# Performance work log

Hardware: AMD Instinct MI355X
Metric: run time of the kernel (lower is better)

## Reference

```python
import jax, jax.numpy as jnp
import numpy as np

NUM_HEADS = 8
HIDDEN_DIM = 64
N_REAL = 30000
N_VIRT = 2000
N_NODES = N_REAL + N_VIRT
N_EDGES = 512000
VOCAB = 100000


def setup_inputs() -> dict:
    key = jax.random.key(0)
    k1, k2, k3, k4, k5 = jax.random.split(key, 5)
    features = jax.random.normal(k1, (VOCAB, HIDDEN_DIM), dtype=jnp.float32)
    virtue_emb = jax.random.normal(k2, (N_VIRT, HIDDEN_DIM), dtype=jnp.float32)  # nn.Embedding weight ~ N(0,1)
    cnodes = jax.random.randint(k3, (N_REAL,), 0, VOCAB, dtype=jnp.int64)
    src = jax.random.randint(k4, (N_EDGES,), 0, N_NODES, dtype=jnp.int64)
    dst = jax.random.randint(k5, (N_EDGES,), 0, N_NODES, dtype=jnp.int64)
    vm_idx = jnp.arange(N_VIRT, dtype=jnp.int64) + N_REAL  # virtual nodes are appended after real nodes
    return {"features": features, "virtue_emb": virtue_emb, "cnodes": cnodes,
            "src": src, "dst": dst, "vm_idx": vm_idx}


def _edge_softmax(e, dst, n_nodes):
    # DGL edge_softmax: softmax over incoming edges of each destination node.
    m = jax.ops.segment_max(e, dst, num_segments=n_nodes)          # [N,H,1]
    ex = jnp.exp(e - m[dst])                                       # [E,H,1]
    s = jax.ops.segment_sum(ex, dst, num_segments=n_nodes)        # [N,H,1]
    return ex / s[dst]


def reference(features, virtue_emb, cnodes, src, dst, vm_idx):
    real_ndata = features[cnodes]                                  # [R,D] F.embedding
    ndata = jnp.concatenate([real_ndata, virtue_emb], axis=0)      # [N,D]
    n = ndata.shape[0]
    # agg_type='neighbor': cat([h]*H, dim=1).view(-1,H,D) == broadcast along head dim
    nft = jnp.broadcast_to(ndata[:, None, :], (n, NUM_HEADS, HIDDEN_DIM))
    e = jnp.ones((src.shape[0], NUM_HEADS, 1), dtype=ndata.dtype)
    eft = _edge_softmax(e, dst, n)                                 # [E,H,1]
    new_nft = jax.ops.segment_sum(nft[src] * eft, dst, num_segments=n)      # round 1: u_mul_e / sum
    final_nft = jax.ops.segment_sum(new_nft[src] * eft, dst, num_segments=n)  # round 2
    return final_nft[vm_idx]                                       # [V,H,D]
```

## Files before the change

### kernel.cpp

```cpp
#include <hip/hip_runtime.h>

constexpr int HEADS  = 8;
constexpr int DIM    = 64;
constexpr int NREAL  = 30000;
constexpr int NVIRT  = 2000;
constexpr int NNODES = NREAL + NVIRT;
constexpr int NEDGES = 512000;
constexpr int STRIDE = 64;

typedef _Float16 half4 __attribute__((ext_vector_type(4)));


__global__ __launch_bounds__(256) void k_prep(const float* __restrict__ features,
                                              const float* __restrict__ virtue,
                                              const int* __restrict__ cnodes,
                                              const int* __restrict__ src,
                                              const int* __restrict__ dst,
                                              _Float16* __restrict__ ndata,
                                              int* __restrict__ cnt,
                                              unsigned char* __restrict__ mark,
                                              unsigned short* __restrict__ slots) {
  int i = blockIdx.x * blockDim.x + threadIdx.x;
  {
    int node = i >> 4;
    int q    = i & 15;
    const float4* srcp = (node < NREAL)
        ? (const float4*)(features + (long)cnodes[node] * DIM)
        : (const float4*)(virtue + (long)(node - NREAL) * DIM);
    float4 v = srcp[q];
    half4 h = { (_Float16)v.x, (_Float16)v.y, (_Float16)v.z, (_Float16)v.w };
    ((half4*)(ndata + (long)node * DIM))[q] = h;
  }
  {
    int d = dst[i];
    int s = src[i];
    int pos = atomicAdd(&cnt[d], 1);
    if (pos < STRIDE) slots[(long)d * STRIDE + pos] = (unsigned short)s;
    if (d >= NREAL) mark[s] = 1;
  }
}

__global__ __launch_bounds__(256) void k_agg1(const int* __restrict__ cnt,
                                              const unsigned char* __restrict__ mark,
                                              const unsigned short* __restrict__ slots,
                                              const _Float16* __restrict__ ndata,
                                              float* __restrict__ new_nft) {
  int node = blockIdx.x * 4 + (threadIdx.x >> 6);
  if (node >= NNODES) return;
  if (!mark[node]) return;
  int lane = threadIdx.x & 63;
  int q = lane >> 4;
  int l = lane & 15;
  int deg = cnt[node];
  if (deg > STRIDE) deg = STRIDE;
  int myidx = 0;
  if (lane < deg) myidx = (int)slots[(long)node * STRIDE + lane];
  float4 acc  = make_float4(0.f, 0.f, 0.f, 0.f);
  float4 acc2 = make_float4(0.f, 0.f, 0.f, 0.f);
  const half4* nd = (const half4*)ndata;
  for (int k0 = 0; k0 < deg; k0 += 8) {
    int ka = k0 + q;
    int kb = k0 + q + 4;
    int sa = __shfl(myidx, ka);
    int sb = __shfl(myidx, kb);
    if (ka < deg) {
      half4 v = nd[(long)sa * 16 + l];
      acc.x += (float)v.x; acc.y += (float)v.y; acc.z += (float)v.z; acc.w += (float)v.w;
    }
    if (kb < deg) {
      half4 v = nd[(long)sb * 16 + l];
      acc2.x += (float)v.x; acc2.y += (float)v.y; acc2.z += (float)v.z; acc2.w += (float)v.w;
    }
  }
  acc.x += acc2.x; acc.y += acc2.y; acc.z += acc2.z; acc.w += acc2.w;
  acc.x += __shfl_xor(acc.x, 16); acc.y += __shfl_xor(acc.y, 16);
  acc.z += __shfl_xor(acc.z, 16); acc.w += __shfl_xor(acc.w, 16);
  acc.x += __shfl_xor(acc.x, 32); acc.y += __shfl_xor(acc.y, 32);
  acc.z += __shfl_xor(acc.z, 32); acc.w += __shfl_xor(acc.w, 32);
  if (q == 0) {
    float inv = (deg > 0) ? 1.0f / (float)deg : 0.0f;
    acc.x *= inv; acc.y *= inv; acc.z *= inv; acc.w *= inv;
    ((float4*)new_nft)[(long)node * 16 + l] = acc;
  }
}

__global__ __launch_bounds__(256) void k_agg2(const int* __restrict__ cnt,
                                              const unsigned short* __restrict__ slots,
                                              const float* __restrict__ new_nft,
                                              float* __restrict__ out) {
  int v = blockIdx.x * 4 + (threadIdx.x >> 6);
  if (v >= NVIRT) return;
  int node = NREAL + v;
  int lane = threadIdx.x & 63;
  int q = lane >> 4;
  int l = lane & 15;
  int deg = cnt[node];
  if (deg > STRIDE) deg = STRIDE;
  int myidx = 0;
  if (lane < deg) myidx = (int)slots[(long)node * STRIDE + lane];
  float4 acc  = make_float4(0.f, 0.f, 0.f, 0.f);
  float4 acc2 = make_float4(0.f, 0.f, 0.f, 0.f);
  const float4* nf4 = (const float4*)new_nft;
  for (int k0 = 0; k0 < deg; k0 += 8) {
    int ka = k0 + q;
    int kb = k0 + q + 4;
    int sa = __shfl(myidx, ka);
    int sb = __shfl(myidx, kb);
    if (ka < deg) {
      float4 x = nf4[(long)sa * 16 + l];
      acc.x += x.x; acc.y += x.y; acc.z += x.z; acc.w += x.w;
    }
    if (kb < deg) {
      float4 x = nf4[(long)sb * 16 + l];
      acc2.x += x.x; acc2.y += x.y; acc2.z += x.z; acc2.w += x.w;
    }
  }
  acc.x += acc2.x; acc.y += acc2.y; acc.z += acc2.z; acc.w += acc2.w;
  acc.x += __shfl_xor(acc.x, 16); acc.y += __shfl_xor(acc.y, 16);
  acc.z += __shfl_xor(acc.z, 16); acc.w += __shfl_xor(acc.w, 16);
  acc.x += __shfl_xor(acc.x, 32); acc.y += __shfl_xor(acc.y, 32);
  acc.z += __shfl_xor(acc.z, 32); acc.w += __shfl_xor(acc.w, 32);
  if (q == 0) {
    float inv = (deg > 0) ? 1.0f / (float)deg : 0.0f;
    acc.x *= inv; acc.y *= inv; acc.z *= inv; acc.w *= inv;
    float4* o4 = (float4*)out;
#pragma unroll
    for (int h = 0; h < HEADS; ++h)
      o4[((long)v * HEADS + h) * 16 + l] = acc;
  }
}


extern "C" void kernel_launch(void* const* d_in, const int* in_sizes, int n_in,
                              void* d_out, int out_size, void* d_ws, size_t ws_size,
                              hipStream_t stream) {
  const float* features = (const float*)d_in[0];
  const float* virtue   = (const float*)d_in[1];
  const int*   cnodes   = (const int*)d_in[2];
  const int*   src      = (const int*)d_in[3];
  const int*   dst      = (const int*)d_in[4];
  float* out = (float*)d_out;

  float*          new_nft = (float*)d_ws;
  _Float16*       ndata   = (_Float16*)(new_nft + (long)NNODES * DIM);
  int*            cnt     = (int*)(ndata + (long)NNODES * DIM);
  unsigned char*  mark    = (unsigned char*)(cnt + NNODES);
  unsigned short* slots   = (unsigned short*)(mark + NNODES);

  const int B = 256;

  hipMemsetAsync(cnt, 0, NNODES * sizeof(int) + NNODES, stream);
  k_prep<<<NEDGES / B, B, 0, stream>>>(features, virtue, cnodes, src, dst,
                                       ndata, cnt, mark, slots);
  k_agg1<<<(NNODES + 3) / 4, B, 0, stream>>>(cnt, mark, slots, ndata, new_nft);
  k_agg2<<<(NVIRT + 3) / 4, B, 0, stream>>>(cnt, slots, new_nft, out);
}
```

Measured before the change: 128.8 us.

## Fuse memset and three kernels into one cooperative persistent kernel

Replaces the memset and three separate launches with a single cooperative kernel of 1024 blocks that uses grid-wide syncs between the zeroing, prep/bucketing, first-aggregation and second-aggregation phases, with grid-stride loops in each phase. This removes launch overhead and the gaps between kernels. In exchange it adds three grid barriers, limits parallelism to a fixed resident grid, and makes the cooperative launch depend on all blocks being co-resident.

```diff
diff --git a/kernel.cpp b/kernel.cpp
--- a/kernel.cpp
+++ b/kernel.cpp
@@ -1,4 +1,7 @@
 #include <hip/hip_runtime.h>
+#include <hip/hip_cooperative_groups.h>
+
+namespace cg = cooperative_groups;
 
 constexpr int HEADS  = 8;
 constexpr int DIM    = 64;
@@ -8,125 +11,130 @@
 constexpr int NEDGES = 512000;
 constexpr int STRIDE = 64;
 
+constexpr int GRID = 1024;
+
 typedef _Float16 half4 __attribute__((ext_vector_type(4)));
 
+__global__ __launch_bounds__(256, 4) void k_fused(const float* __restrict__ features,
+                                                  const float* __restrict__ virtue,
+                                                  const int* __restrict__ cnodes,
+                                                  const int* __restrict__ src,
+                                                  const int* __restrict__ dst,
+                                                  _Float16* __restrict__ ndata,
+                                                  int* __restrict__ cnt,
+                                                  unsigned char* __restrict__ mark,
+                                                  unsigned short* __restrict__ slots,
+                                                  float* __restrict__ new_nft,
+                                                  float* __restrict__ out) {
+  cg::grid_group grid = cg::this_grid();
+  const int tid = blockIdx.x * blockDim.x + threadIdx.x;
+  const int nthreads = GRID * 256;
 
-__global__ __launch_bounds__(256) void k_prep(const float* __restrict__ features,
-                                              const float* __restrict__ virtue,
-                                              const int* __restrict__ cnodes,
-                                              const int* __restrict__ src,
-                                              const int* __restrict__ dst,
-                                              _Float16* __restrict__ ndata,
-                                              int* __restrict__ cnt,
-                                              unsigned char* __restrict__ mark,
-                                              unsigned short* __restrict__ slots) {
-  int i = blockIdx.x * blockDim.x + threadIdx.x;
-  {
-    int node = i >> 4;
-    int q    = i & 15;
-    const float4* srcp = (node < NREAL)
-        ? (const float4*)(features + (long)cnodes[node] * DIM)
-        : (const float4*)(virtue + (long)(node - NREAL) * DIM);
-    float4 v = srcp[q];
-    half4 h = { (_Float16)v.x, (_Float16)v.y, (_Float16)v.z, (_Float16)v.w };
-    ((half4*)(ndata + (long)node * DIM))[q] = h;
+  for (int i = tid; i < NNODES; i += nthreads) {
+    cnt[i] = 0;
+    mark[i] = 0;
   }
-  {
-    int d = dst[i];
-    int s = src[i];
-    int pos = atomicAdd(&cnt[d], 1);
-    if (pos < STRIDE) slots[(long)d * STRIDE + pos] = (unsigned short)s;
-    if (d >= NREAL) mark[s] = 1;
-  }
-}
+  grid.sync();
 
-__global__ __launch_bounds__(256) void k_agg1(const int* __restrict__ cnt,
-                                              const unsigned char* __restrict__ mark,
-                                              const unsigned short* __restrict__ slots,
-                                              const _Float16* __restrict__ ndata,
-                                              float* __restrict__ new_nft) {
-  int node = blockIdx.x * 4 + (threadIdx.x >> 6);
-  if (node >= NNODES) return;
-  if (!mark[node]) return;
-  int lane = threadIdx.x & 63;
-  int q = lane >> 4;
-  int l = lane & 15;
-  int deg = cnt[node];
-  if (deg > STRIDE) deg = STRIDE;
-  int myidx = 0;
-  if (lane < deg) myidx = (int)slots[(long)node * STRIDE + lane];
-  float4 acc  = make_float4(0.f, 0.f, 0.f, 0.f);
-  float4 acc2 = make_float4(0.f, 0.f, 0.f, 0.f);
-  const half4* nd = (const half4*)ndata;
-  for (int k0 = 0; k0 < deg; k0 += 8) {
-    int ka = k0 + q;
-    int kb = k0 + q + 4;
-    int sa = __shfl(myidx, ka);
-    int sb = __shfl(myidx, kb);
-    if (ka < deg) {
-      half4 v = nd[(long)sa * 16 + l];
-      acc.x += (float)v.x; acc.y += (float)v.y; acc.z += (float)v.z; acc.w += (float)v.w;
+  for (int i = tid; i < NEDGES; i += nthreads) {
+    {
+      int node = i >> 4;
+      int q    = i & 15;
+      const float4* srcp = (node < NREAL)
+          ? (const float4*)(features + (long)cnodes[node] * DIM)
+          : (const float4*)(virtue + (long)(node - NREAL) * DIM);
+      float4 v = srcp[q];
+      half4 h = { (_Float16)v.x, (_Float16)v.y, (_Float16)v.z, (_Float16)v.w };
+      ((half4*)(ndata + (long)node * DIM))[q] = h;
     }
-    if (kb < deg) {
-      half4 v = nd[(long)sb * 16 + l];
-      acc2.x += (float)v.x; acc2.y += (float)v.y; acc2.z += (float)v.z; acc2.w += (float)v.w;
+    {
+      int d = dst[i];
+      int s = src[i];
+      int pos = atomicAdd(&cnt[d], 1);
+      if (pos < STRIDE) slots[(long)d * STRIDE + pos] = (unsigned short)s;
+      if (d >= NREAL) mark[s] = 1;
     }
   }
-  acc.x += acc2.x; acc.y += acc2.y; acc.z += acc2.z; acc.w += acc2.w;
-  acc.x += __shfl_xor(acc.x, 16); acc.y += __shfl_xor(acc.y, 16);
-  acc.z += __shfl_xor(acc.z, 16); acc.w += __shfl_xor(acc.w, 16);
-  acc.x += __shfl_xor(acc.x, 32); acc.y += __shfl_xor(acc.y, 32);
-  acc.z += __shfl_xor(acc.z, 32); acc.w += __shfl_xor(acc.w, 32);
-  if (q == 0) {
-    float inv = (deg > 0) ? 1.0f / (float)deg : 0.0f;
-    acc.x *= inv; acc.y *= inv; acc.z *= inv; acc.w *= inv;
-    ((float4*)new_nft)[(long)node * 16 + l] = acc;
-  }
-}
+  grid.sync();
 
-__global__ __launch_bounds__(256) void k_agg2(const int* __restrict__ cnt,
-                                              const unsigned short* __restrict__ slots,
-                                              const float* __restrict__ new_nft,
-                                              float* __restrict__ out) {
-  int v = blockIdx.x * 4 + (threadIdx.x >> 6);
-  if (v >= NVIRT) return;
-  int node = NREAL + v;
-  int lane = threadIdx.x & 63;
-  int q = lane >> 4;
-  int l = lane & 15;
-  int deg = cnt[node];
-  if (deg > STRIDE) deg = STRIDE;
-  int myidx = 0;
-  if (lane < deg) myidx = (int)slots[(long)node * STRIDE + lane];
-  float4 acc  = make_float4(0.f, 0.f, 0.f, 0.f);
-  float4 acc2 = make_float4(0.f, 0.f, 0.f, 0.f);
-  const float4* nf4 = (const float4*)new_nft;
-  for (int k0 = 0; k0 < deg; k0 += 8) {
-    int ka = k0 + q;
-    int kb = k0 + q + 4;
-    int sa = __shfl(myidx, ka);
-    int sb = __shfl(myidx, kb);
-    if (ka < deg) {
-      float4 x = nf4[(long)sa * 16 + l];
-      acc.x += x.x; acc.y += x.y; acc.z += x.z; acc.w += x.w;
+  const int wave   = tid >> 6;
+  const int nwaves = nthreads >> 6;
+  const int lane   = threadIdx.x & 63;
+  const int q = lane >> 4;
+  const int l = lane & 15;
+
+  for (int node = wave; node < NNODES; node += nwaves) {
+    if (!mark[node]) continue;
+    int deg = cnt[node];
+    if (deg > STRIDE) deg = STRIDE;
+    int myidx = 0;
+    if (lane < deg) myidx = (int)slots[(long)node * STRIDE + lane];
+    float4 acc  = make_float4(0.f, 0.f, 0.f, 0.f);
+    float4 acc2 = make_float4(0.f, 0.f, 0.f, 0.f);
+    const half4* nd = (const half4*)ndata;
+    for (int k0 = 0; k0 < deg; k0 += 8) {
+      int ka = k0 + q;
+      int kb = k0 + q + 4;
+      int sa = __shfl(myidx, ka);
+      int sb = __shfl(myidx, kb);
+      if (ka < deg) {
+        half4 v = nd[(long)sa * 16 + l];
+        acc.x += (float)v.x; acc.y += (float)v.y; acc.z += (float)v.z; acc.w += (float)v.w;
+      }
+      if (kb < deg) {
+        half4 v = nd[(long)sb * 16 + l];
+        acc2.x += (float)v.x; acc2.y += (float)v.y; acc2.z += (float)v.z; acc2.w += (float)v.w;
+      }
     }
-    if (kb < deg) {
-      float4 x = nf4[(long)sb * 16 + l];
-      acc2.x += x.x; acc2.y += x.y; acc2.z += x.z; acc2.w += x.w;
+    acc.x += acc2.x; acc.y += acc2.y; acc.z += acc2.z; acc.w += acc2.w;
+    acc.x += __shfl_xor(acc.x, 16); acc.y += __shfl_xor(acc.y, 16);
+    acc.z += __shfl_xor(acc.z, 16); acc.w += __shfl_xor(acc.w, 16);
+    acc.x += __shfl_xor(acc.x, 32); acc.y += __shfl_xor(acc.y, 32);
+    acc.z += __shfl_xor(acc.z, 32); acc.w += __shfl_xor(acc.w, 32);
+    if (q == 0) {
+      float inv = (deg > 0) ? 1.0f / (float)deg : 0.0f;
+      acc.x *= inv; acc.y *= inv; acc.z *= inv; acc.w *= inv;
+      ((float4*)new_nft)[(long)node * 16 + l] = acc;
     }
   }
-  acc.x += acc2.x; acc.y += acc2.y; acc.z += acc2.z; acc.w += acc2.w;
-  acc.x += __shfl_xor(acc.x, 16); acc.y += __shfl_xor(acc.y, 16);
-  acc.z += __shfl_xor(acc.z, 16); acc.w += __shfl_xor(acc.w, 16);
-  acc.x += __shfl_xor(acc.x, 32); acc.y += __shfl_xor(acc.y, 32);
-  acc.z += __shfl_xor(acc.z, 32); acc.w += __shfl_xor(acc.w, 32);
-  if (q == 0) {
-    float inv = (deg > 0) ? 1.0f / (float)deg : 0.0f;
-    acc.x *= inv; acc.y *= inv; acc.z *= inv; acc.w *= inv;
-    float4* o4 = (float4*)out;
+  grid.sync();
+
+  for (int v = wave; v < NVIRT; v += nwaves) {
+    int node = NREAL + v;
+    int deg = cnt[node];
+    if (deg > STRIDE) deg = STRIDE;
+    int myidx = 0;
+    if (lane < deg) myidx = (int)slots[(long)node * STRIDE + lane];
+    float4 acc  = make_float4(0.f, 0.f, 0.f, 0.f);
+    float4 acc2 = make_float4(0.f, 0.f, 0.f, 0.f);
+    const float4* nf4 = (const float4*)new_nft;
+    for (int k0 = 0; k0 < deg; k0 += 8) {
+      int ka = k0 + q;
+      int kb = k0 + q + 4;
+      int sa = __shfl(myidx, ka);
+      int sb = __shfl(myidx, kb);
+      if (ka < deg) {
+        float4 x = nf4[(long)sa * 16 + l];
+        acc.x += x.x; acc.y += x.y; acc.z += x.z; acc.w += x.w;
+      }
+      if (kb < deg) {
+        float4 x = nf4[(long)sb * 16 + l];
+        acc2.x += x.x; acc2.y += x.y; acc2.z += x.z; acc2.w += x.w;
+      }
+    }
+    acc.x += acc2.x; acc.y += acc2.y; acc.z += acc2.z; acc.w += acc2.w;
+    acc.x += __shfl_xor(acc.x, 16); acc.y += __shfl_xor(acc.y, 16);
+    acc.z += __shfl_xor(acc.z, 16); acc.w += __shfl_xor(acc.w, 16);
+    acc.x += __shfl_xor(acc.x, 32); acc.y += __shfl_xor(acc.y, 32);
+    acc.z += __shfl_xor(acc.z, 32); acc.w += __shfl_xor(acc.w, 32);
+    if (q == 0) {
+      float inv = (deg > 0) ? 1.0f / (float)deg : 0.0f;
+      acc.x *= inv; acc.y *= inv; acc.z *= inv; acc.w *= inv;
+      float4* o4 = (float4*)out;
 #pragma unroll
-    for (int h = 0; h < HEADS; ++h)
-      o4[((long)v * HEADS + h) * 16 + l] = acc;
+      for (int h = 0; h < HEADS; ++h)
+        o4[((long)v * HEADS + h) * 16 + l] = acc;
+    }
   }
 }
 
@@ -147,11 +155,8 @@
   unsigned char*  mark    = (unsigned char*)(cnt + NNODES);
   unsigned short* slots   = (unsigned short*)(mark + NNODES);
 
-  const int B = 256;
-
-  hipMemsetAsync(cnt, 0, NNODES * sizeof(int) + NNODES, stream);
-  k_prep<<<NEDGES / B, B, 0, stream>>>(features, virtue, cnodes, src, dst,
-                                       ndata, cnt, mark, slots);
-  k_agg1<<<(NNODES + 3) / 4, B, 0, stream>>>(cnt, mark, slots, ndata, new_nft);
-  k_agg2<<<(NVIRT + 3) / 4, B, 0, stream>>>(cnt, slots, new_nft, out);
+  void* args[] = { (void*)&features, (void*)&virtue, (void*)&cnodes, (void*)&src,
+                   (void*)&dst, (void*)&ndata, (void*)&cnt, (void*)&mark,
+                   (void*)&slots, (void*)&new_nft, (void*)&out };
+  hipLaunchCooperativeKernel((void*)k_fused, dim3(GRID), dim3(256), args, 0, stream);
 }
```

Measured after the change: 430.8 us. 3.34x slower.
